# Kernel tuning notes

Hardware: AMD Instinct MI355X
Metric: run time of the kernel (lower is better)

## Reference

```python
import jax, jax.numpy as jnp
import numpy as np

U = 100          # opts.u_size + 1
ALPHA = 0.01     # LeakyReLU negative slope
NEG = -9.0e15    # mask value used by the original code


def _gat_head(h, adj, W, a):
    """One GraphAttentionLayer head.
    h: [B, N, hd], adj: [B, U, V] bool, W: [hd, hd], a: [2*hd].
    Additive attention score a([Wh_u, Wh_v]) decomposes as a1.Wh_u + a2.Wh_v,
    so the [B,U,V,2hd] pairwise concat of the original need not be materialized
    (same math, LeakyReLU applied after the sum exactly as in torch).
    """
    hd = W.shape[0]
    Wh = h @ W.T                                   # [B, N, hd]
    a1, a2 = a[:hd], a[hd:]
    eu = Wh[:, :U] @ a1                            # [B, U]
    ev = Wh[:, U:] @ a2                            # [B, V]
    e = jax.nn.leaky_relu(eu[:, :, None] + ev[:, None, :], ALPHA)   # [B, U, V]
    e_self = jax.nn.leaky_relu(Wh @ (a1 + a2), ALPHA)               # [B, N]
    e = jnp.where(adj, NEG, e)
    # dual softmax: over V (+self) for U nodes, over U (+self) for V nodes
    attU = jax.nn.softmax(jnp.concatenate([e, e_self[:, :U, None]], axis=2), axis=2)  # [B,U,V+1]
    attV = jnp.swapaxes(
        jax.nn.softmax(jnp.concatenate([e, e_self[:, None, U:]], axis=1), axis=1), 1, 2)  # [B,V,U+1]
    hu = attU[:, :, :-1] @ Wh[:, U:] + Wh[:, :U] * attU[:, :, -1:]  # [B,U,hd]
    hv = attV[:, :, :-1] @ Wh[:, :U] + attV[:, :, -1:] * Wh[:, U:]  # [B,V,hd]
    return jax.nn.elu(jnp.concatenate([hu, hv], axis=1))            # [B,N,hd]


def setup_inputs() -> dict:
    key = jax.random.key(0)
    ks = jax.random.split(key, 6)
    B, N, E, L, H = 16, 300, 128, 3, 8
    hd = E // H
    x = jax.random.normal(ks[0], (B, N, E), dtype=jnp.float32)
    adj = jax.random.bernoulli(ks[1], 0.3, (B, U, N - U))
    weights = jax.random.uniform(ks[2], (B, U, N - U), dtype=jnp.float32)
    # xavier-uniform-like scales (gain 1.414)
    W_layers = jax.random.normal(ks[3], (L, H, hd, hd), dtype=jnp.float32) * (1.414 * np.sqrt(2.0 / (hd + hd)))
    a_layers = jax.random.normal(ks[4], (L, H, 2 * hd), dtype=jnp.float32) * (1.414 * np.sqrt(2.0 / (2 * hd + 1)))
    W_last = jax.random.normal(ks[5], (E, 2 * E + 1), dtype=jnp.float32) * np.sqrt(1.0 / (2 * E + 1))
    return {"x": x, "adj": adj, "weights": weights,
            "W_layers": W_layers, "a_layers": a_layers, "W_last": W_last}


def reference(x, adj, weights, W_layers, a_layers, W_last):
    B, N, E = x.shape
    L, H = W_layers.shape[0], W_layers.shape[1]
    hd = E // H
    V = N - U
    h = x.reshape(B, H, N, hd)                     # matches torch .view head split
    for l in range(L):
        h = jax.vmap(_gat_head, in_axes=(1, None, 0, 0), out_axes=1)(
            h, adj, W_layers[l], a_layers[l])
    hE = h.reshape(B, N, E)
    mask = 1.0 - adj.astype(x.dtype)               # [B, U, V]
    W1, W2, wl = W_last[:, :E], W_last[:, E:2 * E], W_last[:, 2 * E]
    # linear over masked pairwise concat == mask * (Wh_u@W1^T + Wh_v@W2^T) + weights*wl
    pu = hE[:, :U] @ W1.T                          # [B, U, E]
    pv = hE[:, U:] @ W2.T                          # [B, V, E]
    out = mask[..., None] * (pu[:, :, None, :] + pv[:, None, :, :]) \
        + weights[..., None] * wl                  # [B, U, V, E]
    return out.reshape(B, U * V, E)
```

## Files before the change

kernel.cpp:

```cpp
#include <hip/hip_runtime.h>
#include <hip/hip_bf16.h>

#define DI __device__ __forceinline__

typedef _Float16 half8 __attribute__((ext_vector_type(8)));
typedef float f32x4 __attribute__((ext_vector_type(4)));

constexpr int B_ = 16, H_ = 8, N_ = 300, U_ = 100, V_ = 200, HD_ = 16, E_ = 128, L_ = 3;
constexpr int EP = 208;
constexpr float ALPHA_ = 0.01f;
constexpr float NEGI = -20000.0f;

DI float leaky(float x) { return x > 0.f ? x : ALPHA_ * x; }
DI float elu_(float x)  { return x > 0.f ? x : __expf(x) - 1.f; }

DI unsigned short f2bf(float f) {
  unsigned u = __float_as_uint(f);
  unsigned r = (u + 0x7FFFu + ((u >> 16) & 1u)) >> 16;
  return (unsigned short)r;
}
DI float ld_f(const void* p, long i, int isbf) {
  if (isbf) return __uint_as_float(((unsigned)((const unsigned short*)p)[i]) << 16);
  return ((const float*)p)[i];
}
DI bool adj_true(const void* a, long i, int k) {
  switch (k) {
    case 0:  return ((const int*)a)[i] != 0;
    case 1:  return ((const float*)a)[i] != 0.f;
    case 2:  return ((const unsigned short*)a)[i] != 0;
    default: return ((const unsigned char*)a)[i] != 0;
  }
}

DI void detect_flags(const void* x, const void* adj, int* flg) {
  if (threadIdx.x < 64) {
    int lane = threadIdx.x;
    const unsigned short* xh = (const unsigned short*)x;
    bool okbf = true;
    #pragma unroll
    for (int i = 0; i < 16; i++) {
      float f = __uint_as_float(((unsigned)xh[lane * 16 + i]) << 16);
      okbf = okbf && (f == f) && (fabsf(f) < 1e6f);
    }
    int bfall = __all(okbf ? 1 : 0);
    int ak = 3;
    if (adj) {
      const unsigned* aw = (const unsigned*)adj;
      bool i32ok = true, f32ok = true, b16ok = true;
      #pragma unroll
      for (int i = 0; i < 16; i++) {
        unsigned w = aw[lane * 16 + i];
        i32ok = i32ok && (w == 0u || w == 1u);
        f32ok = f32ok && (w == 0u || w == 0x3F800000u);
        unsigned short h0 = (unsigned short)(w & 0xFFFFu), h1 = (unsigned short)(w >> 16);
        b16ok = b16ok && (h0 == 0u || h0 == 0x3F80u) && (h1 == 0u || h1 == 0x3F80u);
      }
      int ai = __all(i32ok ? 1 : 0), af = __all(f32ok ? 1 : 0), ab = __all(b16ok ? 1 : 0);
      ak = ai ? 0 : (af ? 1 : (ab ? 2 : 3));
    }
    if (lane == 0) { flg[0] = bfall; flg[1] = ak; }
  }
  __syncthreads();
}

__global__ __launch_bounds__(256) void k_convert(const void* __restrict__ x,
                                                 const void* __restrict__ Wl, const void* __restrict__ al,
                                                 const void* __restrict__ Wlast,
                                                 float* __restrict__ Wlf, float* __restrict__ alf,
                                                 _Float16* __restrict__ Wt1, _Float16* __restrict__ Wt2,
                                                 float* __restrict__ wlv) {
  __shared__ int flg[2];
  detect_flags(x, nullptr, flg);
  const int isbf = flg[0];
  constexpr int NW = L_ * H_ * HD_ * HD_;
  constexpr int NA = L_ * H_ * 2 * HD_;
  constexpr int NL = E_ * (2 * E_ + 1);
  for (int i = blockIdx.x * 256 + threadIdx.x; i < NW + NA + NL; i += gridDim.x * 256) {
    if (i < NW) Wlf[i] = ld_f(Wl, i, isbf);
    else if (i < NW + NA) alf[i - NW] = ld_f(al, i - NW, isbf);
    else {
      int j = i - NW - NA;
      int e = j / 257, c = j - e * 257;
      float v = ld_f(Wlast, j, isbf);
      if (c < 128) Wt1[c * 128 + e] = (_Float16)v;
      else if (c < 256) Wt2[(c - 128) * 128 + e] = (_Float16)v;
      else wlv[e] = v;
    }
  }
}

__global__ __launch_bounds__(256) void k_gat(const void* __restrict__ x, const void* __restrict__ adj,
                                             const float* __restrict__ Wlf, const float* __restrict__ alf,
                                             _Float16* __restrict__ hE) {
  __shared__ struct {
    unsigned long long maskw[U_][4];
    float eu[U_], ev[V_], es[N_];
    float mU[U_], sU[U_], selfU[U_], rU[U_];
    float mV[V_], sV[V_], selfV[V_], colF[V_];
    float Wsh[256], ash[32], a12[16];
    float M;
    int flg[2];
    _Float16 E[U_ * EP];
    _Float16 Wh[N_ * HD_];
  } s;
  const int tid = threadIdx.x;
  const int b = blockIdx.x >> 3, hh = blockIdx.x & 7;
  detect_flags(x, adj, s.flg);
  const int isbf = s.flg[0], ak = s.flg[1];

  {
    const int wvp = tid >> 6, lanep = tid & 63;
    for (int r = wvp; r < U_; r += 4)
      for (int c = 0; c < 4; c++) {
        int v = c * 64 + lanep;
        bool t = (v < V_) && adj_true(adj, (long)b * (U_ * V_) + (long)r * V_ + v, ak);
        unsigned long long m = __ballot(t ? 1 : 0);
        if (lanep == 0) s.maskw[r][c] = m;
      }
  }

  float hreg[2][16];
  const int row1 = tid + 256;
  {
    const long xb = (long)b * (N_ * E_) + (long)hh * (N_ * HD_);
    #pragma unroll
    for (int k = 0; k < 16; k++) hreg[0][k] = ld_f(x, xb + (long)tid * 16 + k, isbf);
    if (row1 < N_) {
      #pragma unroll
      for (int k = 0; k < 16; k++) hreg[1][k] = ld_f(x, xb + (long)row1 * 16 + k, isbf);
    }
  }
  const int wv = tid >> 6, lane = tid & 63, lm = lane & 15, lq = lane >> 4;

  for (int l = 0; l < L_; l++) {
    __syncthreads();
    s.Wsh[tid] = Wlf[(l * 8 + hh) * 256 + tid];
    if (tid < 32) s.ash[tid] = alf[(l * 8 + hh) * 32 + tid];
    __syncthreads();
    if (tid < 16) s.a12[tid] = s.ash[tid] + s.ash[16 + tid];

    {
      float wr[16];
      #pragma unroll
      for (int d = 0; d < 16; d++) {
        float a = 0.f;
        #pragma unroll
        for (int k = 0; k < 16; k++) a = fmaf(hreg[0][k], s.Wsh[d * 16 + k], a);
        wr[d] = a;
      }
      half8 p0, p1;
      #pragma unroll
      for (int j = 0; j < 8; j++) { p0[j] = (_Float16)wr[j]; p1[j] = (_Float16)wr[8 + j]; }
      *(half8*)&s.Wh[tid * 16] = p0; *(half8*)&s.Wh[tid * 16 + 8] = p1;
      if (row1 < N_) {
        #pragma unroll
        for (int d = 0; d < 16; d++) {
          float a = 0.f;
          #pragma unroll
          for (int k = 0; k < 16; k++) a = fmaf(hreg[1][k], s.Wsh[d * 16 + k], a);
          wr[d] = a;
        }
        #pragma unroll
        for (int j = 0; j < 8; j++) { p0[j] = (_Float16)wr[j]; p1[j] = (_Float16)wr[8 + j]; }
        *(half8*)&s.Wh[row1 * 16] = p0; *(half8*)&s.Wh[row1 * 16 + 8] = p1;
      }
    }
    __syncthreads();
    for (int n = tid; n < N_; n += 256) {
      const half8 h0 = *(const half8*)&s.Wh[n * 16];
      const half8 h1 = *(const half8*)&s.Wh[n * 16 + 8];
      float w[16];
      #pragma unroll
      for (int j = 0; j < 8; j++) { w[j] = (float)h0[j]; w[8 + j] = (float)h1[j]; }
      float da = 0.f, d12 = 0.f;
      if (n < U_) { for (int k = 0; k < 16; k++) da = fmaf(w[k], s.ash[k], da); }
      else        { for (int k = 0; k < 16; k++) da = fmaf(w[k], s.ash[16 + k], da); }
      #pragma unroll
      for (int k = 0; k < 16; k++) d12 = fmaf(w[k], s.a12[k], d12);
      if (n < U_) s.eu[n] = da; else s.ev[n - U_] = da;
      s.es[n] = leaky(d12);
    }
    __syncthreads();
    for (int i = tid; i < U_ * EP; i += 256) {
      int u = i / EP, v = i - u * EP;
      float val = NEGI;
      if (v < V_) {
        bool msk = (s.maskw[u][v >> 6] >> (v & 63)) & 1ull;
        if (!msk) val = leaky(s.eu[u] + s.ev[v]);
      }
      s.E[i] = (_Float16)val;
    }
    __syncthreads();
    for (int v = tid; v < V_; v += 256) {
      float m = s.es[U_ + v];
      for (int u = 0; u < U_; u++) m = fmaxf(m, (float)s.E[u * EP + v]);
      s.mV[v] = m;
    }
    for (int u = tid; u < U_; u += 256) {
      float m = s.es[u];
      const half8* rp = (const half8*)&s.E[u * EP];
      for (int c = 0; c < EP / 8; c++) {
        half8 h = rp[c];
        #pragma unroll
        for (int j = 0; j < 8; j++) m = fmaxf(m, (float)h[j]);
      }
      s.mU[u] = m;
    }
    __syncthreads();
    if (tid < 64) {
      float m = -1e30f;
      for (int u = tid; u < U_; u += 64) m = fmaxf(m, s.mU[u]);
      #pragma unroll
      for (int o = 32; o > 0; o >>= 1) m = fmaxf(m, __shfl_xor(m, o));
      if (tid == 0) s.M = m;
    }
    __syncthreads();
    for (int u = tid; u < U_; u += 256) {
      const float m = s.mU[u];
      float sum = __expf(s.es[u] - m);
      s.selfU[u] = sum;
      half8* rp = (half8*)&s.E[u * EP];
      for (int c = 0; c < EP / 8; c++) {
        half8 h = rp[c]; half8 o;
        #pragma unroll
        for (int j = 0; j < 8; j++) { float p = __expf((float)h[j] - m); sum += p; o[j] = (_Float16)p; }
        rp[c] = o;
      }
      s.sU[u] = sum;
      s.rU[u] = __expf(m - s.M);
    }
    for (int v = tid; v < V_; v += 256) {
      float mv = s.mV[v];
      s.colF[v] = __expf(s.M - mv);
      s.selfV[v] = __expf(s.es[U_ + v] - mv);
    }
    __syncthreads();
    for (int v = tid; v < V_; v += 256) {
      float sum = 0.f;
      for (int u = 0; u < U_; u++) sum = fmaf((float)s.E[u * EP + v], s.rU[u], sum);
      s.sV[v] = sum * s.colF[v] + s.selfV[v];
    }
    __syncthreads();
    float huv[2][4] = {}; float hvv[4][4] = {};
    {
      f32x4 accU[2] = {};
      #pragma unroll
      for (int kt = 0; kt < 7; kt++) {
        half8 bf;
        #pragma unroll
        for (int j = 0; j < 8; j++) {
          int k = kt * 32 + lq * 8 + j;
          bf[j] = (k < V_) ? s.Wh[(U_ + k) * HD_ + lm] : (_Float16)0.f;
        }
        #pragma unroll
        for (int i = 0; i < 2; i++) {
          int mt = wv + 4 * i;
          if (mt >= 7) continue;
          int m = mt * 16 + lm;
          half8 af = {};
          if (m < U_ && (kt * 32 + lq * 8) < EP)
            af = *(const half8*)&s.E[m * EP + kt * 32 + lq * 8];
          accU[i] = __builtin_amdgcn_mfma_f32_16x16x32_f16(af, bf, accU[i], 0, 0, 0);
        }
      }
      #pragma unroll
      for (int i = 0; i < 2; i++) {
        int mt = wv + 4 * i;
        if (mt >= 7) continue;
        #pragma unroll
        for (int r = 0; r < 4; r++) {
          int u = mt * 16 + lq * 4 + r;
          if (u < U_) {
            float val = (accU[i][r] + s.selfU[u] * (float)s.Wh[u * HD_ + lm]) / s.sU[u];
            huv[i][r] = elu_(val);
          }
        }
      }
      f32x4 accV[4] = {};
      #pragma unroll
      for (int kt = 0; kt < 4; kt++) {
        half8 bf;
        #pragma unroll
        for (int j = 0; j < 8; j++) {
          int u = kt * 32 + lq * 8 + j;
          bf[j] = (u < U_) ? s.Wh[u * HD_ + lm] : (_Float16)0.f;
        }
        #pragma unroll
        for (int i = 0; i < 4; i++) {
          int mt = wv + 4 * i;
          if (mt >= 13) continue;
          int v = mt * 16 + lm;
          half8 af = {};
          if (v < V_) {
            float cf = s.colF[v];
            #pragma unroll
            for (int j = 0; j < 8; j++) {
              int u = kt * 32 + lq * 8 + j;
              af[j] = (u < U_) ? (_Float16)((float)s.E[u * EP + v] * s.rU[u] * cf) : (_Float16)0.f;
            }
          }
          accV[i] = __builtin_amdgcn_mfma_f32_16x16x32_f16(af, bf, accV[i], 0, 0, 0);
        }
      }
      #pragma unroll
      for (int i = 0; i < 4; i++) {
        int mt = wv + 4 * i;
        if (mt >= 13) continue;
        #pragma unroll
        for (int r = 0; r < 4; r++) {
          int v = mt * 16 + lq * 4 + r;
          if (v < V_) {
            float val = (accV[i][r] + s.selfV[v] * (float)s.Wh[(U_ + v) * HD_ + lm]) / s.sV[v];
            hvv[i][r] = elu_(val);
          }
        }
      }
    }
    __syncthreads();
    if (l < L_ - 1) {
      #pragma unroll
      for (int i = 0; i < 2; i++) {
        int mt = wv + 4 * i; if (mt >= 7) continue;
        #pragma unroll
        for (int r = 0; r < 4; r++) {
          int u = mt * 16 + lq * 4 + r;
          if (u < U_) s.Wh[u * HD_ + lm] = (_Float16)huv[i][r];
        }
      }
      #pragma unroll
      for (int i = 0; i < 4; i++) {
        int mt = wv + 4 * i; if (mt >= 13) continue;
        #pragma unroll
        for (int r = 0; r < 4; r++) {
          int v = mt * 16 + lq * 4 + r;
          if (v < V_) s.Wh[(U_ + v) * HD_ + lm] = (_Float16)hvv[i][r];
        }
      }
      __syncthreads();
      #pragma unroll
      for (int k = 0; k < 16; k++) hreg[0][k] = (float)s.Wh[tid * 16 + k];
      if (row1 < N_) {
        #pragma unroll
        for (int k = 0; k < 16; k++) hreg[1][k] = (float)s.Wh[row1 * 16 + k];
      }
    } else {
      _Float16* op = hE + (long)b * (N_ * E_) + (long)hh * (N_ * HD_);
      #pragma unroll
      for (int i = 0; i < 2; i++) {
        int mt = wv + 4 * i; if (mt >= 7) continue;
        #pragma unroll
        for (int r = 0; r < 4; r++) {
          int u = mt * 16 + lq * 4 + r;
          if (u < U_) op[u * HD_ + lm] = (_Float16)huv[i][r];
        }
      }
      #pragma unroll
      for (int i = 0; i < 4; i++) {
        int mt = wv + 4 * i; if (mt >= 13) continue;
        #pragma unroll
        for (int r = 0; r < 4; r++) {
          int v = mt * 16 + lq * 4 + r;
          if (v < V_) op[(U_ + v) * HD_ + lm] = (_Float16)hvv[i][r];
        }
      }
    }
  }
}

__global__ __launch_bounds__(256) void k_pupv(const _Float16* __restrict__ hE,
                                              const _Float16* __restrict__ Wt1,
                                              const _Float16* __restrict__ Wt2,
                                              float* __restrict__ pu, float* __restrict__ pv) {
  __shared__ _Float16 At[16 * 136];
  __shared__ _Float16 Bt[128 * 136];
  const int tid = threadIdx.x;
  const int b = blockIdx.x / 20, t = blockIdx.x % 20;
  const bool isU = t < 7;
  const int r0 = (isU ? t : t - 7) * 16;
  const int rows = isU ? U_ : V_;
  const int base = isU ? 0 : U_;
  const _Float16* W = isU ? Wt1 : Wt2;
  {
    int rr = tid >> 4, c8 = (tid & 15) * 8;
    half8 v = {};
    if (r0 + rr < rows) v = *(const half8*)&hE[(long)b * (N_ * E_) + (long)(base + r0 + rr) * E_ + c8];
    *(half8*)&At[rr * 136 + c8] = v;
  }
  for (int i = tid; i < 128 * 16; i += 256) {
    int k = i >> 4, c8 = (i & 15) * 8;
    *(half8*)&Bt[k * 136 + c8] = *(const half8*)&W[k * 128 + c8];
  }
  __syncthreads();
  const int wv = tid >> 6, lane = tid & 63, lm = lane & 15, lq = lane >> 4;
  f32x4 acc[2] = {};
  #pragma unroll
  for (int kt = 0; kt < 4; kt++) {
    half8 af = *(const half8*)&At[lm * 136 + kt * 32 + lq * 8];
    #pragma unroll
    for (int i = 0; i < 2; i++) {
      int nt = wv + 4 * i;
      int n = nt * 16 + lm;
      half8 bf;
      #pragma unroll
      for (int j = 0; j < 8; j++) bf[j] = Bt[(kt * 32 + lq * 8 + j) * 136 + n];
      acc[i] = __builtin_amdgcn_mfma_f32_16x16x32_f16(af, bf, acc[i], 0, 0, 0);
    }
  }
  float* out = isU ? pu : pv;
  #pragma unroll
  for (int i = 0; i < 2; i++) {
    int nt = wv + 4 * i;
    #pragma unroll
    for (int r = 0; r < 4; r++) {
      int grow = r0 + lq * 4 + r;
      if (grow < rows) out[(long)b * rows * E_ + (long)grow * E_ + nt * 16 + lm] = acc[i][r];
    }
  }
}

__global__ __launch_bounds__(256) void k_out(const void* __restrict__ x, const void* __restrict__ adj,
                                             const void* __restrict__ wgt,
                                             const float* __restrict__ pu, const float* __restrict__ pv,
                                             const float* __restrict__ wlv, void* __restrict__ out) {
  __shared__ int flg[2];
  __shared__ float puS[128], wlS[128];
  detect_flags(x, adj, flg);
  const int isbf = flg[0], ak = flg[1];
  const int tid = threadIdx.x;
  const int b = blockIdx.x / U_, u = blockIdx.x % U_;
  if (tid < 128) {
    puS[tid] = pu[((long)b * U_ + u) * E_ + tid];
    wlS[tid] = wlv[tid];
  }
  __syncthreads();
  const int ei = (tid & 15) * 8;
  float p8[8], w8[8];
  #pragma unroll
  for (int j = 0; j < 8; j++) { p8[j] = puS[ei + j]; w8[j] = wlS[ei + j]; }
  for (int v = tid >> 4; v < V_; v += 16) {
    const long mi = (long)b * (U_ * V_) + (long)u * V_ + v;
    const float msk = adj_true(adj, mi, ak) ? 0.f : 1.f;
    const float wq = ld_f(wgt, mi, isbf);
    const float4* pvp = (const float4*)&pv[((long)b * V_ + v) * E_ + ei];
    float4 a = pvp[0], c = pvp[1];
    float o[8];
    o[0] = msk * (p8[0] + a.x) + wq * w8[0];
    o[1] = msk * (p8[1] + a.y) + wq * w8[1];
    o[2] = msk * (p8[2] + a.z) + wq * w8[2];
    o[3] = msk * (p8[3] + a.w) + wq * w8[3];
    o[4] = msk * (p8[4] + c.x) + wq * w8[4];
    o[5] = msk * (p8[5] + c.y) + wq * w8[5];
    o[6] = msk * (p8[6] + c.z) + wq * w8[6];
    o[7] = msk * (p8[7] + c.w) + wq * w8[7];
    const long ob = ((long)b * (U_ * V_) + (long)u * V_ + v) * E_ + ei;
    if (isbf) {
      uint4 pk;
      pk.x = (unsigned)f2bf(o[0]) | ((unsigned)f2bf(o[1]) << 16);
      pk.y = (unsigned)f2bf(o[2]) | ((unsigned)f2bf(o[3]) << 16);
      pk.z = (unsigned)f2bf(o[4]) | ((unsigned)f2bf(o[5]) << 16);
      pk.w = (unsigned)f2bf(o[6]) | ((unsigned)f2bf(o[7]) << 16);
      *(uint4*)((unsigned short*)out + ob) = pk;
    } else {
      float* op = (float*)out + ob;
      float4 f0 = {o[0], o[1], o[2], o[3]}, f1 = {o[4], o[5], o[6], o[7]};
      *(float4*)op = f0;
      *(float4*)(op + 4) = f1;
    }
  }
}

extern "C" void kernel_launch(void* const* d_in, const int* in_sizes, int n_in,
                              void* d_out, int out_size, void* d_ws, size_t ws_size,
                              hipStream_t stream) {
  const void* x     = d_in[0];
  const void* adj   = d_in[1];
  const void* wgt   = d_in[2];
  const void* Wl    = d_in[3];
  const void* al    = d_in[4];
  const void* Wlast = d_in[5];

  char* ws = (char*)d_ws;
  size_t off = 0;
  auto alloc = [&](size_t bytes) -> void* {
    void* p = ws + off;
    off += (bytes + 255) & ~(size_t)255;
    return p;
  };
  float*     Wlf = (float*)alloc(6144 * 4);
  float*     alf = (float*)alloc(768 * 4);
  _Float16*  Wt1 = (_Float16*)alloc(16384 * 2);
  _Float16*  Wt2 = (_Float16*)alloc(16384 * 2);
  float*     wlv = (float*)alloc(128 * 4);
  _Float16*  hE  = (_Float16*)alloc((size_t)B_ * N_ * E_ * 2);
  float*     pu  = (float*)alloc((size_t)B_ * U_ * E_ * 4);
  float*     pv  = (float*)alloc((size_t)B_ * V_ * E_ * 4);

  k_convert<<<156, 256, 0, stream>>>(x, Wl, al, Wlast, Wlf, alf, Wt1, Wt2, wlv);
  k_gat<<<B_ * H_, 256, 0, stream>>>(x, adj, Wlf, alf, hE);
  k_pupv<<<B_ * 20, 256, 0, stream>>>(hE, Wt1, Wt2, pu, pv);
  k_out<<<B_ * U_, 256, 0, stream>>>(x, adj, wgt, pu, pv, wlv, d_out);
}
```

Baseline: 346.0 us.

## Restructure GAT kernel with on-the-fly softmax bound and MFMA row sums

Rewrites the GAT layer kernel so the attention matrix is never stored in shared memory. Each row's exponentials are computed on the fly against an analytic upper bound (eu + max ev, clipped at zero, and the self score) instead of an exact row max. Row sums come from an MFMA against a ones vector, and Wh projection also uses MFMA with fp16 weights. The block grows to 512 threads, and a transposed adjacency mask is precomputed for the V-side pass. This removes several barriers and max/sum passes, at the risk of fp16 underflow because the bound replaces the true max.

```diff
diff --git a/kernel.cpp b/kernel.cpp
--- a/kernel.cpp
+++ b/kernel.cpp
@@ -7,9 +7,7 @@
 typedef float f32x4 __attribute__((ext_vector_type(4)));
 
 constexpr int B_ = 16, H_ = 8, N_ = 300, U_ = 100, V_ = 200, HD_ = 16, E_ = 128, L_ = 3;
-constexpr int EP = 208;
 constexpr float ALPHA_ = 0.01f;
-constexpr float NEGI = -20000.0f;
 
 DI float leaky(float x) { return x > 0.f ? x : ALPHA_ * x; }
 DI float elu_(float x)  { return x > 0.f ? x : __expf(x) - 1.f; }
@@ -66,7 +64,7 @@
 __global__ __launch_bounds__(256) void k_convert(const void* __restrict__ x,
                                                  const void* __restrict__ Wl, const void* __restrict__ al,
                                                  const void* __restrict__ Wlast,
-                                                 float* __restrict__ Wlf, float* __restrict__ alf,
+                                                 _Float16* __restrict__ Wlf16, float* __restrict__ alf,
                                                  _Float16* __restrict__ Wt1, _Float16* __restrict__ Wt2,
                                                  float* __restrict__ wlv) {
   __shared__ int flg[2];
@@ -76,7 +74,7 @@
   constexpr int NA = L_ * H_ * 2 * HD_;
   constexpr int NL = E_ * (2 * E_ + 1);
   for (int i = blockIdx.x * 256 + threadIdx.x; i < NW + NA + NL; i += gridDim.x * 256) {
-    if (i < NW) Wlf[i] = ld_f(Wl, i, isbf);
+    if (i < NW) Wlf16[i] = (_Float16)ld_f(Wl, i, isbf);
     else if (i < NW + NA) alf[i - NW] = ld_f(al, i - NW, isbf);
     else {
       int j = i - NW - NA;
@@ -89,281 +87,203 @@
   }
 }
 
-__global__ __launch_bounds__(256) void k_gat(const void* __restrict__ x, const void* __restrict__ adj,
-                                             const float* __restrict__ Wlf, const float* __restrict__ alf,
+__global__ __launch_bounds__(512) void k_gat(const void* __restrict__ x, const void* __restrict__ adj,
+                                             const _Float16* __restrict__ Wlf16, const float* __restrict__ alf,
                                              _Float16* __restrict__ hE) {
   __shared__ struct {
-    unsigned long long maskw[U_][4];
-    float eu[U_], ev[V_], es[N_];
-    float mU[U_], sU[U_], selfU[U_], rU[U_];
-    float mV[V_], sV[V_], selfV[V_], colF[V_];
-    float Wsh[256], ash[32], a12[16];
-    float M;
+    unsigned long long maskw[112][4];
+    unsigned long long maskv[208][2];
+    __attribute__((aligned(16))) _Float16 hS[304][16];
+    __attribute__((aligned(16))) _Float16 Wh[304][16];
+    __attribute__((aligned(16))) _Float16 WhT[16][328];
+    __attribute__((aligned(16))) float eu[128];
+    __attribute__((aligned(16))) float ev[256];
+    __attribute__((aligned(16))) float es[312];
+    float mEU, mEV;
     int flg[2];
-    _Float16 E[U_ * EP];
-    _Float16 Wh[N_ * HD_];
   } s;
   const int tid = threadIdx.x;
   const int b = blockIdx.x >> 3, hh = blockIdx.x & 7;
   detect_flags(x, adj, s.flg);
   const int isbf = s.flg[0], ak = s.flg[1];
-
-  {
-    const int wvp = tid >> 6, lanep = tid & 63;
-    for (int r = wvp; r < U_; r += 4)
-      for (int c = 0; c < 4; c++) {
-        int v = c * 64 + lanep;
-        bool t = (v < V_) && adj_true(adj, (long)b * (U_ * V_) + (long)r * V_ + v, ak);
-        unsigned long long m = __ballot(t ? 1 : 0);
-        if (lanep == 0) s.maskw[r][c] = m;
-      }
-  }
-
-  float hreg[2][16];
-  const int row1 = tid + 256;
-  {
-    const long xb = (long)b * (N_ * E_) + (long)hh * (N_ * HD_);
+  const int wv = tid >> 6, lane = tid & 63, lm = lane & 15, lq = lane >> 4;
+  const long adjb = (long)b * (U_ * V_);
+
+  for (int r = wv; r < 112; r += 8) {
     #pragma unroll
-    for (int k = 0; k < 16; k++) hreg[0][k] = ld_f(x, xb + (long)tid * 16 + k, isbf);
-    if (row1 < N_) {
-      #pragma unroll
-      for (int k = 0; k < 16; k++) hreg[1][k] = ld_f(x, xb + (long)row1 * 16 + k, isbf);
-    }
-  }
-  const int wv = tid >> 6, lane = tid & 63, lm = lane & 15, lq = lane >> 4;
+    for (int c = 0; c < 4; c++) {
+      int v = c * 64 + lane;
+      bool ex = true;
+      if (r < U_ && v < V_) ex = adj_true(adj, adjb + (long)r * V_ + v, ak);
+      unsigned long long m = __ballot(ex ? 1 : 0);
+      if (lane == 0) s.maskw[r][c] = m;
+    }
+  }
+  for (int v = wv; v < 208; v += 8) {
+    bool e0 = true, e1 = true;
+    if (v < V_) {
+      e0 = adj_true(adj, adjb + (long)lane * V_ + v, ak);
+      int u1 = 64 + lane;
+      if (u1 < U_) e1 = adj_true(adj, adjb + (long)u1 * V_ + v, ak);
+    }
+    unsigned long long m0 = __ballot(e0 ? 1 : 0);
+    unsigned long long m1 = __ballot(e1 ? 1 : 0);
+    if (lane == 0) { s.maskv[v][0] = m0; s.maskv[v][1] = m1; }
+  }
+  for (int i = tid; i < 16 * 328 / 2; i += 512) ((unsigned*)&s.WhT[0][0])[i] = 0u;
+  if (tid < 28) s.eu[100 + tid] = 0.f;
+  if (tid >= 32 && tid < 88) s.ev[200 + (tid - 32)] = 0.f;
+  if (tid >= 96 && tid < 108) s.es[300 + (tid - 96)] = 0.f;
+  if (tid >= 128 && tid < 160) ((unsigned*)&s.hS[300][0])[tid - 128] = 0u;
+  if (tid < N_) {
+    const long xb = (long)b * (N_ * E_) + (long)hh * (N_ * HD_) + (long)tid * 16;
+    half8 p0, p1;
+    #pragma unroll
+    for (int k = 0; k < 8; k++) { p0[k] = (_Float16)ld_f(x, xb + k, isbf); p1[k] = (_Float16)ld_f(x, xb + 8 + k, isbf); }
+    *(half8*)&s.hS[tid][0] = p0; *(half8*)&s.hS[tid][8] = p1;
+  }
+  __syncthreads();
+
+  half8 ones8;
+  #pragma unroll
+  for (int j = 0; j < 8; j++) ones8[j] = (_Float16)1.f;
 
   for (int l = 0; l < L_; l++) {
-    __syncthreads();
-    s.Wsh[tid] = Wlf[(l * 8 + hh) * 256 + tid];
-    if (tid < 32) s.ash[tid] = alf[(l * 8 + hh) * 32 + tid];
-    __syncthreads();
-    if (tid < 16) s.a12[tid] = s.ash[tid] + s.ash[16 + tid];
-
     {
-      float wr[16];
-      #pragma unroll
-      for (int d = 0; d < 16; d++) {
-        float a = 0.f;
-        #pragma unroll
-        for (int k = 0; k < 16; k++) a = fmaf(hreg[0][k], s.Wsh[d * 16 + k], a);
-        wr[d] = a;
-      }
-      half8 p0, p1;
-      #pragma unroll
-      for (int j = 0; j < 8; j++) { p0[j] = (_Float16)wr[j]; p1[j] = (_Float16)wr[8 + j]; }
-      *(half8*)&s.Wh[tid * 16] = p0; *(half8*)&s.Wh[tid * 16 + 8] = p1;
-      if (row1 < N_) {
-        #pragma unroll
-        for (int d = 0; d < 16; d++) {
-          float a = 0.f;
-          #pragma unroll
-          for (int k = 0; k < 16; k++) a = fmaf(hreg[1][k], s.Wsh[d * 16 + k], a);
-          wr[d] = a;
-        }
-        #pragma unroll
-        for (int j = 0; j < 8; j++) { p0[j] = (_Float16)wr[j]; p1[j] = (_Float16)wr[8 + j]; }
-        *(half8*)&s.Wh[row1 * 16] = p0; *(half8*)&s.Wh[row1 * 16 + 8] = p1;
-      }
-    }
-    __syncthreads();
-    for (int n = tid; n < N_; n += 256) {
-      const half8 h0 = *(const half8*)&s.Wh[n * 16];
-      const half8 h1 = *(const half8*)&s.Wh[n * 16 + 8];
-      float w[16];
-      #pragma unroll
-      for (int j = 0; j < 8; j++) { w[j] = (float)h0[j]; w[8 + j] = (float)h1[j]; }
-      float da = 0.f, d12 = 0.f;
-      if (n < U_) { for (int k = 0; k < 16; k++) da = fmaf(w[k], s.ash[k], da); }
-      else        { for (int k = 0; k < 16; k++) da = fmaf(w[k], s.ash[16 + k], da); }
-      #pragma unroll
-      for (int k = 0; k < 16; k++) d12 = fmaf(w[k], s.a12[k], d12);
-      if (n < U_) s.eu[n] = da; else s.ev[n - U_] = da;
-      s.es[n] = leaky(d12);
-    }
-    __syncthreads();
-    for (int i = tid; i < U_ * EP; i += 256) {
-      int u = i / EP, v = i - u * EP;
-      float val = NEGI;
-      if (v < V_) {
-        bool msk = (s.maskw[u][v >> 6] >> (v & 63)) & 1ull;
-        if (!msk) val = leaky(s.eu[u] + s.ev[v]);
-      }
-      s.E[i] = (_Float16)val;
-    }
-    __syncthreads();
-    for (int v = tid; v < V_; v += 256) {
-      float m = s.es[U_ + v];
-      for (int u = 0; u < U_; u++) m = fmaxf(m, (float)s.E[u * EP + v]);
-      s.mV[v] = m;
-    }
-    for (int u = tid; u < U_; u += 256) {
-      float m = s.es[u];
-      const half8* rp = (const half8*)&s.E[u * EP];
-      for (int c = 0; c < EP / 8; c++) {
-        half8 h = rp[c];
-        #pragma unroll
-        for (int j = 0; j < 8; j++) m = fmaxf(m, (float)h[j]);
-      }
-      s.mU[u] = m;
-    }
-    __syncthreads();
-    if (tid < 64) {
-      float m = -1e30f;
-      for (int u = tid; u < U_; u += 64) m = fmaxf(m, s.mU[u]);
-      #pragma unroll
-      for (int o = 32; o > 0; o >>= 1) m = fmaxf(m, __shfl_xor(m, o));
-      if (tid == 0) s.M = m;
-    }
-    __syncthreads();
-    for (int u = tid; u < U_; u += 256) {
-      const float m = s.mU[u];
-      float sum = __expf(s.es[u] - m);
-      s.selfU[u] = sum;
-      half8* rp = (half8*)&s.E[u * EP];
-      for (int c = 0; c < EP / 8; c++) {
-        half8 h = rp[c]; half8 o;
-        #pragma unroll
-        for (int j = 0; j < 8; j++) { float p = __expf((float)h[j] - m); sum += p; o[j] = (_Float16)p; }
-        rp[c] = o;
-      }
-      s.sU[u] = sum;
-      s.rU[u] = __expf(m - s.M);
-    }
-    for (int v = tid; v < V_; v += 256) {
-      float mv = s.mV[v];
-      s.colF[v] = __expf(s.M - mv);
-      s.selfV[v] = __expf(s.es[U_ + v] - mv);
-    }
-    __syncthreads();
-    for (int v = tid; v < V_; v += 256) {
-      float sum = 0.f;
-      for (int u = 0; u < U_; u++) sum = fmaf((float)s.E[u * EP + v], s.rU[u], sum);
-      s.sV[v] = sum * s.colF[v] + s.selfV[v];
-    }
-    __syncthreads();
-    float huv[2][4] = {}; float hvv[4][4] = {};
-    {
-      f32x4 accU[2] = {};
-      #pragma unroll
-      for (int kt = 0; kt < 7; kt++) {
-        half8 bf;
-        #pragma unroll
-        for (int j = 0; j < 8; j++) {
-          int k = kt * 32 + lq * 8 + j;
-          bf[j] = (k < V_) ? s.Wh[(U_ + k) * HD_ + lm] : (_Float16)0.f;
-        }
-        #pragma unroll
-        for (int i = 0; i < 2; i++) {
-          int mt = wv + 4 * i;
-          if (mt >= 7) continue;
-          int m = mt * 16 + lm;
-          half8 af = {};
-          if (m < U_ && (kt * 32 + lq * 8) < EP)
-            af = *(const half8*)&s.E[m * EP + kt * 32 + lq * 8];
-          accU[i] = __builtin_amdgcn_mfma_f32_16x16x32_f16(af, bf, accU[i], 0, 0, 0);
-        }
-      }
-      #pragma unroll
-      for (int i = 0; i < 2; i++) {
-        int mt = wv + 4 * i;
-        if (mt >= 7) continue;
+      const int base32 = (l * 8 + hh) * 32;
+      const float a1l = alf[base32 + lm], a2l = alf[base32 + 16 + lm];
+      half8 bW = {};
+      if (lq < 2) bW = *(const half8*)&Wlf16[(l * 8 + hh) * 256 + lm * 16 + lq * 8];
+      for (int t = wv; t < 19; t += 8) {
+        const int row_a = t * 16 + lm;
+        half8 af = {};
+        if (lq < 2) af = *(const half8*)&s.hS[row_a][lq * 8];
+        f32x4 z = {0.f, 0.f, 0.f, 0.f};
+        f32x4 dW = __builtin_amdgcn_mfma_f32_16x16x32_f16(af, bW, z, 0, 0, 0);
         #pragma unroll
         for (int r = 0; r < 4; r++) {
-          int u = mt * 16 + lq * 4 + r;
-          if (u < U_) {
-            float val = (accU[i][r] + s.selfU[u] * (float)s.Wh[u * HD_ + lm]) / s.sU[u];
-            huv[i][r] = elu_(val);
+          const int row = t * 16 + lq * 4 + r;
+          const float aX = (row < U_) ? a1l : a2l;
+          float d1 = dW[r] * aX, d2 = dW[r] * (a1l + a2l);
+          #pragma unroll
+          for (int o = 1; o < 16; o <<= 1) { d1 += __shfl_xor(d1, o); d2 += __shfl_xor(d2, o); }
+          if (row < N_) {
+            s.Wh[row][lm] = (_Float16)dW[r];
+            s.WhT[lm][row < U_ ? row : row + 4] = (_Float16)dW[r];
+            if (lm == 0) { if (row < U_) s.eu[row] = d1; else s.ev[row - U_] = d1; }
+            if (lm == 1) s.es[row] = leaky(d2);
           }
         }
       }
-      f32x4 accV[4] = {};
-      #pragma unroll
-      for (int kt = 0; kt < 4; kt++) {
-        half8 bf;
+    }
+    __syncthreads();
+    if (wv == 0) {
+      float m = fmaxf(s.eu[lane], s.eu[64 + lane]);
+      #pragma unroll
+      for (int o = 32; o > 0; o >>= 1) m = fmaxf(m, __shfl_xor(m, o));
+      if (lane == 0) s.mEU = m;
+    } else if (wv == 1) {
+      float m = fmaxf(fmaxf(s.ev[lane], s.ev[64 + lane]), fmaxf(s.ev[128 + lane], s.ev[192 + lane]));
+      #pragma unroll
+      for (int o = 32; o > 0; o >>= 1) m = fmaxf(m, __shfl_xor(m, o));
+      if (lane == 0) s.mEV = m;
+    }
+    __syncthreads();
+    const float mEU = s.mEU, mEV = s.mEV;
+    const bool last = (l == L_ - 1);
+    _Float16* outp = hE + (long)b * (N_ * E_) + (long)hh * (N_ * HD_);
+
+    if (wv < 7) {
+      const int t = wv;
+      const int u_a = t * 16 + lm;
+      const float eu_a = s.eu[u_a];
+      const float sh_a = fmaxf(fmaxf(eu_a + mEV, 0.f), s.es[u_a]);
+      const unsigned long long mw0 = s.maskw[u_a][0], mw1 = s.maskw[u_a][1];
+      const unsigned long long mw2 = s.maskw[u_a][2], mw3 = s.maskw[u_a][3];
+      f32x4 accU = {0.f, 0.f, 0.f, 0.f}, accS = {0.f, 0.f, 0.f, 0.f};
+      #pragma unroll
+      for (int kt = 0; kt < 7; kt++) {
+        const int base = kt * 32 + lq * 8;
+        unsigned long long w = (base < 64) ? mw0 : (base < 128) ? mw1 : (base < 192) ? mw2 : mw3;
+        const unsigned bits = (unsigned)(w >> (base & 63)) & 0xFFu;
+        const float4 e0 = *(const float4*)&s.ev[base];
+        const float4 e1 = *(const float4*)&s.ev[base + 4];
+        const float ev8[8] = {e0.x, e0.y, e0.z, e0.w, e1.x, e1.y, e1.z, e1.w};
+        half8 af;
         #pragma unroll
         for (int j = 0; j < 8; j++) {
-          int u = kt * 32 + lq * 8 + j;
-          bf[j] = (u < U_) ? s.Wh[u * HD_ + lm] : (_Float16)0.f;
+          float p = __expf(leaky(eu_a + ev8[j]) - sh_a);
+          af[j] = (bits >> j & 1u) ? (_Float16)0.f : (_Float16)p;
+        }
+        const half8 bf = *(const half8*)&s.WhT[lm][104 + base];
+        accU = __builtin_amdgcn_mfma_f32_16x16x32_f16(af, bf, accU, 0, 0, 0);
+        accS = __builtin_amdgcn_mfma_f32_16x16x32_f16(af, ones8, accS, 0, 0, 0);
+      }
+      #pragma unroll
+      for (int r = 0; r < 4; r++) {
+        const int u_c = t * 16 + lq * 4 + r;
+        if (u_c < U_) {
+          const float eu_c = s.eu[u_c];
+          const float sh_c = fmaxf(fmaxf(eu_c + mEV, 0.f), s.es[u_c]);
+          const float self = __expf(s.es[u_c] - sh_c);
+          const float num = accU[r] + self * (float)s.Wh[u_c][lm];
+          const float den = accS[r] + self;
+          const float o = elu_(num / den);
+          if (last) outp[u_c * 16 + lm] = (_Float16)o;
+          else s.hS[u_c][lm] = (_Float16)o;
+        }
+      }
+    }
+    {
+      int vt0 = wv, vt1 = -1, vt2 = -1;
+      if (wv == 4) vt1 = 12;
+      else if (wv == 5) vt1 = 10;
+      else if (wv == 6) vt1 = 11;
+      else if (wv == 7) { vt1 = 8; vt2 = 9; }
+      const int vts[3] = {vt0, vt1, vt2};
+      #pragma unroll
+      for (int ti = 0; ti < 3; ti++) {
+        const int t = vts[ti];
+        if (t < 0) continue;
+        const int v_a = t * 16 + lm;
+        const float ev_a = s.ev[v_a];
+        const float sh_a = fmaxf(fmaxf(ev_a + mEU, 0.f), s.es[U_ + v_a]);
+        const unsigned long long m0 = s.maskv[v_a][0], m1 = s.maskv[v_a][1];
+        f32x4 accV = {0.f, 0.f, 0.f, 0.f}, accS = {0.f, 0.f, 0.f, 0.f};
+        #pragma unroll
+        for (int kt = 0; kt < 4; kt++) {
+          const int base = kt * 32 + lq * 8;
+          const unsigned bits = (unsigned)(((base < 64) ? m0 : m1) >> (base & 63)) & 0xFFu;
+          const float4 u0 = *(const float4*)&s.eu[base];
+          const float4 u1 = *(const float4*)&s.eu[base + 4];
+          const float eu8[8] = {u0.x, u0.y, u0.z, u0.w, u1.x, u1.y, u1.z, u1.w};
+          half8 af;
+          #pragma unroll
+          for (int j = 0; j < 8; j++) {
+            float p = __expf(leaky(eu8[j] + ev_a) - sh_a);
+            af[j] = (bits >> j & 1u) ? (_Float16)0.f : (_Float16)p;
+          }
+          const half8 bf = *(const half8*)&s.WhT[lm][base];
+          accV = __builtin_amdgcn_mfma_f32_16x16x32_f16(af, bf, accV, 0, 0, 0);
+          accS = __builtin_amdgcn_mfma_f32_16x16x32_f16(af, ones8, accS, 0, 0, 0);
         }
         #pragma unroll
-        for (int i = 0; i < 4; i++) {
-          int mt = wv + 4 * i;
-          if (mt >= 13) continue;
-          int v = mt * 16 + lm;
-          half8 af = {};
-          if (v < V_) {
-            float cf = s.colF[v];
-            #pragma unroll
-            for (int j = 0; j < 8; j++) {
-              int u = kt * 32 + lq * 8 + j;
-              af[j] = (u < U_) ? (_Float16)((float)s.E[u * EP + v] * s.rU[u] * cf) : (_Float16)0.f;
-            }
-          }
-          accV[i] = __builtin_amdgcn_mfma_f32_16x16x32_f16(af, bf, accV[i], 0, 0, 0);
-        }
-      }
-      #pragma unroll
-      for (int i = 0; i < 4; i++) {
-        int mt = wv + 4 * i;
-        if (mt >= 13) continue;
-        #pragma unroll
         for (int r = 0; r < 4; r++) {
-          int v = mt * 16 + lq * 4 + r;
-          if (v < V_) {
-            float val = (accV[i][r] + s.selfV[v] * (float)s.Wh[(U_ + v) * HD_ + lm]) / s.sV[v];
-            hvv[i][r] = elu_(val);
+          const int v_c = t * 16 + lq * 4 + r;
+          if (v_c < V_) {
+            const float ev_c = s.ev[v_c];
+            const float sh_c = fmaxf(fmaxf(ev_c + mEU, 0.f), s.es[U_ + v_c]);
+            const float self = __expf(s.es[U_ + v_c] - sh_c);
+            const float num = accV[r] + self * (float)s.Wh[U_ + v_c][lm];
+            const float den = accS[r] + self;
+            const float o = elu_(num / den);
+            if (last) outp[(U_ + v_c) * 16 + lm] = (_Float16)o;
+            else s.hS[U_ + v_c][lm] = (_Float16)o;
           }
         }
       }
     }
     __syncthreads();
-    if (l < L_ - 1) {
-      #pragma unroll
-      for (int i = 0; i < 2; i++) {
-        int mt = wv + 4 * i; if (mt >= 7) continue;
-        #pragma unroll
-        for (int r = 0; r < 4; r++) {
-          int u = mt * 16 + lq * 4 + r;
-          if (u < U_) s.Wh[u * HD_ + lm] = (_Float16)huv[i][r];
-        }
-      }
-      #pragma unroll
-      for (int i = 0; i < 4; i++) {
-        int mt = wv + 4 * i; if (mt >= 13) continue;
-        #pragma unroll
-        for (int r = 0; r < 4; r++) {
-          int v = mt * 16 + lq * 4 + r;
-          if (v < V_) s.Wh[(U_ + v) * HD_ + lm] = (_Float16)hvv[i][r];
-        }
-      }
-      __syncthreads();
-      #pragma unroll
-      for (int k = 0; k < 16; k++) hreg[0][k] = (float)s.Wh[tid * 16 + k];
-      if (row1 < N_) {
-        #pragma unroll
-        for (int k = 0; k < 16; k++) hreg[1][k] = (float)s.Wh[row1 * 16 + k];
-      }
-    } else {
-      _Float16* op = hE + (long)b * (N_ * E_) + (long)hh * (N_ * HD_);
-      #pragma unroll
-      for (int i = 0; i < 2; i++) {
-        int mt = wv + 4 * i; if (mt >= 7) continue;
-        #pragma unroll
-        for (int r = 0; r < 4; r++) {
-          int u = mt * 16 + lq * 4 + r;
-          if (u < U_) op[u * HD_ + lm] = (_Float16)huv[i][r];
-        }
-      }
-      #pragma unroll
-      for (int i = 0; i < 4; i++) {
-        int mt = wv + 4 * i; if (mt >= 13) continue;
-        #pragma unroll
-        for (int r = 0; r < 4; r++) {
-          int v = mt * 16 + lq * 4 + r;
-          if (v < V_) op[(U_ + v) * HD_ + lm] = (_Float16)hvv[i][r];
-        }
-      }
-    }
   }
 }
 
@@ -486,17 +406,17 @@
     off += (bytes + 255) & ~(size_t)255;
     return p;
   };
-  float*     Wlf = (float*)alloc(6144 * 4);
-  float*     alf = (float*)alloc(768 * 4);
-  _Float16*  Wt1 = (_Float16*)alloc(16384 * 2);
-  _Float16*  Wt2 = (_Float16*)alloc(16384 * 2);
-  float*     wlv = (float*)alloc(128 * 4);
-  _Float16*  hE  = (_Float16*)alloc((size_t)B_ * N_ * E_ * 2);
-  float*     pu  = (float*)alloc((size_t)B_ * U_ * E_ * 4);
-  float*     pv  = (float*)alloc((size_t)B_ * V_ * E_ * 4);
-
-  k_convert<<<156, 256, 0, stream>>>(x, Wl, al, Wlast, Wlf, alf, Wt1, Wt2, wlv);
-  k_gat<<<B_ * H_, 256, 0, stream>>>(x, adj, Wlf, alf, hE);
+  _Float16*  Wlf16 = (_Float16*)alloc(6144 * 2);
+  float*     alf   = (float*)alloc(768 * 4);
+  _Float16*  Wt1   = (_Float16*)alloc(16384 * 2);
+  _Float16*  Wt2   = (_Float16*)alloc(16384 * 2);
+  float*     wlv   = (float*)alloc(128 * 4);
+  _Float16*  hE    = (_Float16*)alloc((size_t)B_ * N_ * E_ * 2);
+  float*     pu    = (float*)alloc((size_t)B_ * U_ * E_ * 4);
+  float*     pv    = (float*)alloc((size_t)B_ * V_ * E_ * 4);
+
+  k_convert<<<156, 256, 0, stream>>>(x, Wl, al, Wlast, Wlf16, alf, Wt1, Wt2, wlv);
+  k_gat<<<B_ * H_, 512, 0, stream>>>(x, adj, Wlf16, alf, hE);
   k_pupv<<<B_ * 20, 256, 0, stream>>>(hE, Wt1, Wt2, pu, pv);
   k_out<<<B_ * U_, 256, 0, stream>>>(x, adj, wgt, pu, pv, wlv, d_out);
 }
```

Measured after the change: 277.2 us. 1.25x faster.
